# Kernel tuning notes

Measured on AMD Instinct MI355X. Metric: run time of the kernel, lower is better.

Reference implementation:

```python
import jax, jax.numpy as jnp
import numpy as np

N, E, F_IN, HID, H1, H2, H3, OUT = 10000, 160000, 50, 350, 4, 4, 6, 121


def _gat(x, src, dst, n, W, a_s, a_d, b, heads, C, concat):
    # PyG GATConv (dropout=0, eval): h = xW^T reshaped to [N,H,C]
    h = (x @ W.T).reshape(n, heads, C)
    alpha_src = jnp.einsum('nhc,hc->nh', h, a_s)  # [N,H]
    alpha_dst = jnp.einsum('nhc,hc->nh', h, a_d)  # [N,H]
    e = jax.nn.leaky_relu(alpha_src[src] + alpha_dst[dst], 0.2)  # [E,H]
    # numerically-stable segment softmax over incoming edges of each dst node
    m = jax.ops.segment_max(e, dst, num_segments=n)
    ee = jnp.exp(e - m[dst])
    s = jax.ops.segment_sum(ee, dst, num_segments=n)
    alpha = ee / s[dst]  # self-loops guarantee s > 0
    out = jax.ops.segment_sum(h[src] * alpha[:, :, None], dst, num_segments=n)  # [N,H,C]
    out = out.reshape(n, heads * C) if concat else out.mean(axis=1)
    return out + b


def setup_inputs() -> dict:
    key = jax.random.key(0)
    ks = jax.random.split(key, 16)
    sc = 0.05
    inp = {
        'x': jax.random.normal(ks[0], (N, F_IN), dtype=jnp.float32),
        'edge_index': jax.random.randint(ks[1], (2, E), 0, N, dtype=jnp.int64) if jax.config.jax_enable_x64 else jax.random.randint(ks[1], (2, E), 0, N, dtype=jnp.int32),
        'W1': jax.random.normal(ks[2], (H1 * HID, F_IN), dtype=jnp.float32) * sc,
        'a1s': jax.random.normal(ks[3], (H1, HID), dtype=jnp.float32) * sc,
        'a1d': jax.random.normal(ks[4], (H1, HID), dtype=jnp.float32) * sc,
        'b1': jnp.zeros((H1 * HID,), dtype=jnp.float32),
        'W2': jax.random.normal(ks[5], (H2 * HID, H1 * HID), dtype=jnp.float32) * sc,
        'a2s': jax.random.normal(ks[6], (H2, HID), dtype=jnp.float32) * sc,
        'a2d': jax.random.normal(ks[7], (H2, HID), dtype=jnp.float32) * sc,
        'b2': jnp.zeros((H2 * HID,), dtype=jnp.float32),
        'Wskip': jax.random.normal(ks[8], (H2 * HID, H1 * HID), dtype=jnp.float32) * sc,
        'W3': jax.random.normal(ks[9], (H3 * OUT, H2 * HID), dtype=jnp.float32) * sc,
        'a3s': jax.random.normal(ks[10], (H3, OUT), dtype=jnp.float32) * sc,
        'a3d': jax.random.normal(ks[11], (H3, OUT), dtype=jnp.float32) * sc,
        'b3': jnp.zeros((OUT,), dtype=jnp.float32),
    }
    return inp


def reference(x, edge_index, W1, a1s, a1d, b1, W2, a2s, a2d, b2, Wskip, W3, a3s, a3d, b3):
    n = x.shape[0]
    loops = jnp.arange(n, dtype=edge_index.dtype)  # PyG add_self_loops=True
    src = jnp.concatenate([edge_index[0], loops])
    dst = jnp.concatenate([edge_index[1], loops])
    h = jax.nn.elu(_gat(x, src, dst, n, W1, a1s, a1d, b1, H1, HID, True))
    x_in = h
    h = jax.nn.elu(_gat(h, src, dst, n, W2, a2s, a2d, b2, H2, HID, True))
    h = h + x_in @ Wskip.T  # skip connection (bias=False)
    return _gat(h, src, dst, n, W3, a3s, a3d, b3, H3, OUT, False)
```

## Files before the change

### kernel.cpp

```cpp
#include <hip/hip_runtime.h>
#include <math.h>

#define NNODES 10000
#define NEDGES 160000
#define E2 (NEDGES + NNODES)
#define F_IN 50
#define HIDC 350
#define NH1 4
#define NH2 4
#define NH3 6
#define OUTC 121
#define MAXE 96
#define KP1 64
#define KP2 1408
#define LD3 736
#define ROWSLACK 128

typedef __attribute__((ext_vector_type(8))) short short8;
typedef __attribute__((ext_vector_type(8))) unsigned short ushort8v;
typedef __attribute__((ext_vector_type(4))) float floatx4;

static __device__ __forceinline__ unsigned short f2bf(float f) {
    unsigned u = __float_as_uint(f);
    unsigned r = (u + 0x7fffu + ((u >> 16) & 1u)) >> 16;
    return (unsigned short)r;
}
static __device__ __forceinline__ float bf2f(unsigned short s) {
    return __uint_as_float(((unsigned)s) << 16);
}

#define GLL16(gp, lp)                                                      \
    __builtin_amdgcn_global_load_lds(                                      \
        (const __attribute__((address_space(1))) void*)(gp),               \
        (__attribute__((address_space(3))) void*)(lp), 16, 0, 0)

__global__ void count_kernel(const int* __restrict__ ei, int* __restrict__ cnt) {
    int i = blockIdx.x * blockDim.x + threadIdx.x;
    if (i >= E2) return;
    int dst = (i < NEDGES) ? ei[NEDGES + i] : (i - NEDGES);
    atomicAdd(&cnt[dst], 1);
}

__global__ void scan_kernel(const int* __restrict__ cnt, int* __restrict__ indptr,
                            int* __restrict__ cursor) {
    __shared__ int part[1024];
    int tid = threadIdx.x;
    const int CH = (NNODES + 1023) / 1024;
    int base = tid * CH;
    int s = 0;
    for (int i = 0; i < CH; i++) {
        int idx = base + i;
        if (idx < NNODES) s += cnt[idx];
    }
    part[tid] = s;
    __syncthreads();
    for (int off = 1; off < 1024; off <<= 1) {
        int v = (tid >= off) ? part[tid - off] : 0;
        __syncthreads();
        part[tid] += v;
        __syncthreads();
    }
    int run = (tid == 0) ? 0 : part[tid - 1];
    for (int i = 0; i < CH; i++) {
        int idx = base + i;
        if (idx < NNODES) {
            indptr[idx] = run;
            cursor[idx] = run;
            run += cnt[idx];
        }
    }
    if (tid == 0) indptr[NNODES] = part[1023];
}

__global__ void scatter_kernel(const int* __restrict__ ei, int* __restrict__ cursor,
                               int* __restrict__ esrc) {
    int i = blockIdx.x * blockDim.x + threadIdx.x;
    if (i >= E2) return;
    int src, dst;
    if (i < NEDGES) {
        src = ei[i];
        dst = ei[NEDGES + i];
    } else {
        src = dst = i - NEDGES;
    }
    int pos = atomicAdd(&cursor[dst], 1);
    esrc[pos] = src;
}

__global__ void splitW1_kernel(const float* __restrict__ W1,
                               unsigned short* __restrict__ w1Hi,
                               unsigned short* __restrict__ w1Lo) {
    int k = threadIdx.x;
    int r = blockIdx.x;
    float v = (k < F_IN) ? W1[(size_t)r * F_IN + k] : 0.f;
    unsigned short h = f2bf(v);
    w1Hi[(size_t)r * KP1 + k] = h;
    w1Lo[(size_t)r * KP1 + k] = f2bf(v - bf2f(h));
}

__global__ void splitB_kernel(const float* __restrict__ W2, const float* __restrict__ Wsk,
                              const float* __restrict__ W3,
                              unsigned short* __restrict__ w2Hi,
                              unsigned short* __restrict__ w3Hi) {
    int k = blockIdx.x * blockDim.x + threadIdx.x;
    if (k >= KP2) return;
    int r = blockIdx.y;
    const int K = 1400;
    const float* src;
    unsigned short* hi;
    int row;
    if (r < 1400) { src = W2; row = r; hi = w2Hi; }
    else if (r < 2800) { src = Wsk; row = r - 1400; hi = w2Hi + (size_t)1400 * KP2; }
    else { src = W3; row = r - 2800; hi = w3Hi; }
    float v = (k < K) ? src[(size_t)row * K + k] : 0.f;
    hi[(size_t)row * KP2 + k] = f2bf(v);
}

__global__ void atil_kernel(const float* __restrict__ W, const float* __restrict__ av_s,
                            const float* __restrict__ av_d, float* __restrict__ outS,
                            float* __restrict__ outD, int C, int K, int cchunk) {
    int k = blockIdx.x * 64 + (threadIdx.x & 63);
    if (k >= K) return;
    int h = blockIdx.y;
    int c0 = blockIdx.z * cchunk;
    int c1 = c0 + cchunk;
    if (c1 > C) c1 = C;
    float ss = 0.f, dd = 0.f;
    for (int c = c0; c < c1; c++) {
        float wv = W[((size_t)h * C + c) * K + k];
        ss = fmaf(wv, av_s[h * C + c], ss);
        dd = fmaf(wv, av_d[h * C + c], dd);
    }
    atomicAdd(&outS[(size_t)h * K + k], ss);
    atomicAdd(&outD[(size_t)h * K + k], dd);
}

__global__ void splitAT2_kernel(const float* __restrict__ atall,
                                unsigned short* __restrict__ atHi,
                                unsigned short* __restrict__ atLo) {
    int k = blockIdx.x * 64 + threadIdx.x;
    int r = blockIdx.y;
    float v = 0.f;
    if (k < 1400) {
        if (r < 4) v = atall[400 + r * 1400 + k];
        else if (r < 8) v = atall[6000 + (r - 4) * 1400 + k];
    }
    unsigned short h = f2bf(v);
    atHi[(size_t)r * KP2 + k] = h;
    atLo[(size_t)r * KP2 + k] = f2bf(v - bf2f(h));
}

__global__ __launch_bounds__(256) void alpha1x_kernel(const float* __restrict__ x,
                                                      const float* __restrict__ at1s,
                                                      const float* __restrict__ at1d,
                                                      float* __restrict__ as1,
                                                      float* __restrict__ ad1) {
    int wave = threadIdx.x >> 6, lane = threadIdx.x & 63;
    int n = blockIdx.x * 4 + wave;
    if (n >= NNODES) return;
    int kk = lane < F_IN ? lane : F_IN - 1;
    float v = (lane < F_IN) ? x[(size_t)n * F_IN + lane] : 0.f;
    float p[8];
#pragma unroll
    for (int h = 0; h < 4; h++) {
        p[h] = v * at1s[h * F_IN + kk];
        p[4 + h] = v * at1d[h * F_IN + kk];
    }
#pragma unroll
    for (int s = 0; s < 8; s++)
#pragma unroll
        for (int o = 32; o > 0; o >>= 1) p[s] += __shfl_xor(p[s], o, 64);
    if (lane == 0) {
#pragma unroll
        for (int h = 0; h < 4; h++) {
            as1[n * 4 + h] = p[h];
            ad1[n * 4 + h] = p[4 + h];
        }
    }
}

__global__ void zeropad_kernel(unsigned short* __restrict__ hi) {
    int i = blockIdx.x * 256 + threadIdx.x;
    if (i >= NNODES * 8) return;
    int n = i >> 3, c = 1400 + (i & 7);
    hi[(size_t)n * KP2 + c] = 0;
}

__global__ __launch_bounds__(256) void agg_x(
    const float* __restrict__ x, const float* __restrict__ as_n,
    const float* __restrict__ ad_n, const int* __restrict__ indptr,
    const int* __restrict__ esrc, unsigned short* __restrict__ xaggHi,
    unsigned short* __restrict__ xaggLo) {
    int n = blockIdx.x, tid = threadIdx.x;
    int s = indptr[n], e = indptr[n + 1];
    int deg = e - s;
    if (deg > MAXE) deg = MAXE;
    __shared__ int srcs[MAXE];
    __shared__ float wgt[MAXE * 4];

    if (tid < 64) {
        int lane = tid;
        float adv[4], mx[4], sm[4];
#pragma unroll
        for (int h = 0; h < 4; h++) {
            adv[h] = ad_n[n * 4 + h];
            mx[h] = -1e30f;
            sm[h] = 0.f;
        }
        for (int j = lane; j < deg; j += 64) {
            int sr = esrc[s + j];
            srcs[j] = sr;
#pragma unroll
            for (int h = 0; h < 4; h++) {
                float ev = as_n[sr * 4 + h] + adv[h];
                ev = ev > 0.f ? ev : 0.2f * ev;
                wgt[j * 4 + h] = ev;
                mx[h] = fmaxf(mx[h], ev);
            }
        }
#pragma unroll
        for (int h = 0; h < 4; h++)
#pragma unroll
            for (int o = 32; o > 0; o >>= 1) mx[h] = fmaxf(mx[h], __shfl_xor(mx[h], o, 64));
        for (int j = lane; j < deg; j += 64) {
#pragma unroll
            for (int h = 0; h < 4; h++) {
                float p = __expf(wgt[j * 4 + h] - mx[h]);
                wgt[j * 4 + h] = p;
                sm[h] += p;
            }
        }
#pragma unroll
        for (int h = 0; h < 4; h++) {
#pragma unroll
            for (int o = 32; o > 0; o >>= 1) sm[h] += __shfl_xor(sm[h], o, 64);
            sm[h] = 1.f / sm[h];
        }
        for (int j = lane; j < deg; j += 64) {
#pragma unroll
            for (int h = 0; h < 4; h++) wgt[j * 4 + h] *= sm[h];
        }
    }
    __syncthreads();

    int h = tid >> 6, k = tid & 63;
    float a = 0.f;
    if (k < F_IN) {
        float a2 = 0.f;
        int j = 0;
        for (; j + 1 < deg; j += 2) {
            a = fmaf(wgt[j * 4 + h], x[(size_t)srcs[j] * F_IN + k], a);
            a2 = fmaf(wgt[(j + 1) * 4 + h], x[(size_t)srcs[j + 1] * F_IN + k], a2);
        }
        if (j < deg) a = fmaf(wgt[j * 4 + h], x[(size_t)srcs[j] * F_IN + k], a);
        a += a2;
    }
    unsigned short hi = f2bf(a);
    xaggHi[(size_t)n * 256 + tid] = hi;
    xaggLo[(size_t)n * 256 + tid] = f2bf(a - bf2f(hi));
}

__global__ __launch_bounds__(256, 2) void gemm_h1(
    const unsigned short* __restrict__ xaggHi, const unsigned short* __restrict__ xaggLo,
    const unsigned short* __restrict__ w1Hi, const unsigned short* __restrict__ w1Lo,
    const float* __restrict__ bias, unsigned short* __restrict__ actHi) {
    __shared__ __align__(16) unsigned short sA[2][128 * 32];
    __shared__ __align__(16) unsigned short sB[2][256 * 32];
    int tid = threadIdx.x;
    int wave = tid >> 6, lane = tid & 63;
    int wm = (wave >> 1) * 64, wn = (wave & 1) * 128;
    int fr = lane & 15, kq = lane >> 4;
    int row0 = blockIdx.y * 128, col0 = blockIdx.x * 256;
    int hd = blockIdx.z;

    floatx4 acc[4][8];
#pragma unroll
    for (int i = 0; i < 4; i++)
#pragma unroll
        for (int j = 0; j < 8; j++)
#pragma unroll
            for (int q = 0; q < 4; q++) acc[i][j][q] = 0.f;

    int gpos = lane & 3;
    int rl = lane >> 2;
    int gsw = kq ^ ((fr >> 1) & 3);

    for (int k0 = 0; k0 < 64; k0 += 32) {
#pragma unroll
        for (int c = 0; c < 2; ++c) {
            int r = wave * 32 + c * 16 + rl;
            int g = gpos ^ ((r >> 1) & 3);
            size_t gofs = (size_t)(row0 + r) * 256 + hd * 64 + k0 + g * 8;
            size_t lofs = (size_t)r * 32 + (size_t)gpos * 8;
            GLL16(xaggHi + gofs, &sA[0][lofs]);
            GLL16(xaggLo + gofs, &sA[1][lofs]);
        }
#pragma unroll
        for (int c = 0; c < 4; ++c) {
            int r = wave * 64 + c * 16 + rl;
            int g = gpos ^ ((r >> 1) & 3);
            size_t gofs = (size_t)(hd * 350 + col0 + r) * KP1 + k0 + g * 8;
            size_t lofs = (size_t)r * 32 + (size_t)gpos * 8;
            GLL16(w1Hi + gofs, &sB[0][lofs]);
            GLL16(w1Lo + gofs, &sB[1][lofs]);
        }
        __syncthreads();

        short8 ah[4], al[4], bh[8], bl[8];
#pragma unroll
        for (int j = 0; j < 8; j++) {
            int rb = wn + j * 16 + fr;
            bh[j] = *(const short8*)&sB[0][rb * 32 + gsw * 8];
            bl[j] = *(const short8*)&sB[1][rb * 32 + gsw * 8];
        }
#pragma unroll
        for (int i = 0; i < 4; i++) {
            int ra = wm + i * 16 + fr;
            ah[i] = *(const short8*)&sA[0][ra * 32 + gsw * 8];
            al[i] = *(const short8*)&sA[1][ra * 32 + gsw * 8];
        }
#pragma unroll
        for (int i = 0; i < 4; i++)
#pragma unroll
            for (int j = 0; j < 8; j++) {
                acc[i][j] = __builtin_amdgcn_mfma_f32_16x16x32_bf16(ah[i], bh[j],
                                                                   acc[i][j], 0, 0, 0);
                acc[i][j] = __builtin_amdgcn_mfma_f32_16x16x32_bf16(al[i], bh[j],
                                                                   acc[i][j], 0, 0, 0);
                acc[i][j] = __builtin_amdgcn_mfma_f32_16x16x32_bf16(ah[i], bl[j],
                                                                   acc[i][j], 0, 0, 0);
            }
        __syncthreads();
    }

#pragma unroll
    for (int i = 0; i < 4; i++) {
#pragma unroll
        for (int rg = 0; rg < 4; rg++) {
            int rr = row0 + wm + i * 16 + kq * 4 + rg;
            if (rr >= NNODES) continue;
#pragma unroll
            for (int j = 0; j < 8; j++) {
                int cc = col0 + wn + j * 16 + fr;
                if (cc < 350) {
                    int gc = hd * 350 + cc;
                    float v = acc[i][j][rg] + bias[gc];
                    v = v > 0.f ? v : expm1f(v);
                    actHi[(size_t)rr * KP2 + gc] = f2bf(v);
                }
            }
        }
    }
}

__global__ __launch_bounds__(256) void alpha_mfma(
    const unsigned short* __restrict__ act, const unsigned short* __restrict__ tHi,
    const unsigned short* __restrict__ tLo, int H, float* __restrict__ asx,
    float* __restrict__ adx) {
    int wave = threadIdx.x >> 6, lane = threadIdx.x & 63;
    int row0 = (blockIdx.x * 4 + wave) * 16;
    if (row0 >= NNODES) return;
    int fr = lane & 15, kq = lane >> 4;
    floatx4 acc = {0.f, 0.f, 0.f, 0.f};
    const unsigned short* arow = act + (size_t)(row0 + fr) * KP2 + kq * 8;
    const unsigned short* brh = tHi + (size_t)fr * KP2 + kq * 8;
    const unsigned short* brl = tLo + (size_t)fr * KP2 + kq * 8;
#pragma unroll 4
    for (int k0 = 0; k0 < KP2; k0 += 32) {
        short8 a = *(const short8*)(arow + k0);
        short8 vh = *(const short8*)(brh + k0);
        short8 vl = *(const short8*)(brl + k0);
        acc = __builtin_amdgcn_mfma_f32_16x16x32_bf16(a, vh, acc, 0, 0, 0);
        acc = __builtin_amdgcn_mfma_f32_16x16x32_bf16(a, vl, acc, 0, 0, 0);
    }
#pragma unroll
    for (int rg = 0; rg < 4; rg++) {
        int rr = row0 + kq * 4 + rg;
        if (fr < H) asx[rr * H + fr] = acc[rg];
        else if (fr < 2 * H) adx[rr * H + (fr - H)] = acc[rg];
    }
}

template <int H>
__global__ __launch_bounds__(64) void alpha_edge(
    const float* __restrict__ as_n, const float* __restrict__ ad_n,
    const int* __restrict__ indptr, const int* __restrict__ esrc,
    float* __restrict__ walpha) {
    int n = blockIdx.x;
    int lane = threadIdx.x;
    int s = indptr[n], e = indptr[n + 1];
    int deg = e - s;
    if (deg > MAXE) deg = MAXE;
    __shared__ float wgt[MAXE * H];
    float adv[H], mx[H], sm[H];
#pragma unroll
    for (int h = 0; h < H; h++) {
        adv[h] = ad_n[n * H + h];
        mx[h] = -1e30f;
        sm[h] = 0.f;
    }
    for (int j = lane; j < deg; j += 64) {
        int sr = esrc[s + j];
#pragma unroll
        for (int h = 0; h < H; h++) {
            float ev = as_n[sr * H + h] + adv[h];
            ev = ev > 0.f ? ev : 0.2f * ev;
            wgt[j * H + h] = ev;
            mx[h] = fmaxf(mx[h], ev);
        }
    }
#pragma unroll
    for (int h = 0; h < H; h++)
#pragma unroll
        for (int o = 32; o > 0; o >>= 1) mx[h] = fmaxf(mx[h], __shfl_xor(mx[h], o, 64));
    for (int j = lane; j < deg; j += 64) {
#pragma unroll
        for (int h = 0; h < H; h++) {
            float p = __expf(wgt[j * H + h] - mx[h]);
            wgt[j * H + h] = p;
            sm[h] += p;
        }
    }
#pragma unroll
    for (int h = 0; h < H; h++) {
#pragma unroll
        for (int o = 32; o > 0; o >>= 1) sm[h] += __shfl_xor(sm[h], o, 64);
        sm[h] = 1.f / sm[h];
    }
    for (int j = lane; j < deg; j += 64) {
#pragma unroll
        for (int h = 0; h < H; h++) wgt[j * H + h] *= sm[h];
    }
    __syncthreads();
    for (int i = lane; i < deg * H; i += 64)
        walpha[(size_t)s * H + i] = wgt[i];
}

#define PH_MFMA(CH)                                                          \
    __builtin_amdgcn_s_barrier();                                            \
    asm volatile("s_waitcnt lgkmcnt(0)" ::: "memory");                       \
    __builtin_amdgcn_sched_barrier(0);                                       \
    __builtin_amdgcn_s_setprio(1);                                           \
    _Pragma("unroll")                                                        \
    for (int rf = 0; rf < 4; rf++) {                                         \
        _Pragma("unroll")                                                    \
        for (int cf = 0; cf < 4; cf++)                                       \
            acc[(CH) * 4 + rf][cf] = __builtin_amdgcn_mfma_f32_16x16x32_bf16( \
                a[rf], bfr[cf], acc[(CH) * 4 + rf][cf], 0, 0, 0);            \
    }                                                                        \
    __builtin_amdgcn_s_setprio(0);

__global__ __launch_bounds__(512, 2) void gemm_8p(
    const unsigned short* __restrict__ A, const unsigned short* __restrict__ B,
    unsigned short* __restrict__ Cb, int NN, int M, int Kp, int ldc) {
    __shared__ __align__(16) unsigned short sA[2][256 * 32];
    __shared__ __align__(16) unsigned short sB[2][256 * 32];
    int tid = threadIdx.x;
    int w = tid >> 6, lane = tid & 63;
    int wr = w >> 2, wc = w & 3;
    int fr = lane & 15, kq = lane >> 4;

    int gx = (int)gridDim.x;
    int nwg = gx * (int)gridDim.y;
    int bid = (int)blockIdx.y * gx + (int)blockIdx.x;
    int qq = nwg >> 3, rr8 = nwg & 7;
    int xcd = bid & 7, bdx = bid >> 3;
    int nb = (xcd < rr8) ? xcd * (qq + 1) + bdx : rr8 * (qq + 1) + (xcd - rr8) * qq + bdx;
    int row0 = (nb / gx) * 256, col0 = (nb % gx) * 256;

    floatx4 acc[8][4];
#pragma unroll
    for (int i = 0; i < 8; i++)
#pragma unroll
        for (int j = 0; j < 4; j++)
#pragma unroll
            for (int q = 0; q < 4; q++) acc[i][j][q] = 0.f;

    auto stage = [&](unsigned short* plane, const unsigned short* g, int rbase,
                     int kofs) {
#pragma unroll
        for (int l = 0; l < 2; l++) {
            int ix = l * 512 + tid, row = ix >> 2, sl = ix & 3;
            int gp = sl ^ ((row >> 1) & 3);
            GLL16(g + (size_t)(rbase + row) * Kp + kofs + gp * 8,
                  plane + (size_t)row * 32 + sl * 8);
        }
    };
    auto rdA = [&](const unsigned short* plane, int ch, short8* a) {
#pragma unroll
        for (int rf = 0; rf < 4; rf++) {
            int row = wr * 128 + ch * 64 + rf * 16 + fr;
            a[rf] = *(const short8*)(plane + (size_t)row * 32 +
                                     (size_t)(kq ^ ((row >> 1) & 3)) * 8);
        }
    };
    auto rdB = [&](const unsigned short* plane, short8* b) {
#pragma unroll
        for (int cf = 0; cf < 4; cf++) {
            int row = wc * 64 + cf * 16 + fr;
            b[cf] = *(const short8*)(plane + (size_t)row * 32 +
                                     (size_t)(kq ^ ((row >> 1) & 3)) * 8);
        }
    };

    const int nkt = Kp >> 6;
    stage(sA[0], A, row0, 0);
    stage(sB[0], B, col0, 0);
    stage(sB[1], B, col0, 32);
    asm volatile("s_waitcnt vmcnt(2)" ::: "memory");
    __builtin_amdgcn_sched_barrier(0);
    __builtin_amdgcn_s_barrier();

    short8 a[4], bfr[4];
    for (int t = 0; t < nkt; ++t) {
        int kt = t << 6;
        bool more = (t + 1 < nkt);
        rdA(sA[0], 0, a);
        rdB(sB[0], bfr);
        PH_MFMA(0)
        stage(sA[1], A, row0, kt + 32);
        __builtin_amdgcn_s_barrier();
        rdA(sA[0], 1, a);
        PH_MFMA(1)
        if (more) {
            stage(sB[0], B, col0, kt + 64);
            asm volatile("s_waitcnt vmcnt(2)" ::: "memory");
        } else {
            asm volatile("s_waitcnt vmcnt(0)" ::: "memory");
        }
        __builtin_amdgcn_sched_barrier(0);
        __builtin_amdgcn_s_barrier();
        rdA(sA[1], 0, a);
        rdB(sB[1], bfr);
        PH_MFMA(0)
        if (more) stage(sA[0], A, row0, kt + 64);
        __builtin_amdgcn_s_barrier();
        rdA(sA[1], 1, a);
        PH_MFMA(1)
        if (more) {
            stage(sB[1], B, col0, kt + 96);
            asm volatile("s_waitcnt vmcnt(2)" ::: "memory");
            __builtin_amdgcn_sched_barrier(0);
        }
        __builtin_amdgcn_s_barrier();
    }

#pragma unroll
    for (int ch = 0; ch < 2; ch++) {
#pragma unroll
        for (int rf = 0; rf < 4; rf++) {
#pragma unroll
            for (int rg = 0; rg < 4; rg++) {
                int rrow = row0 + wr * 128 + ch * 64 + rf * 16 + kq * 4 + rg;
                if (rrow >= NN) continue;
#pragma unroll
                for (int cf = 0; cf < 4; cf++) {
                    int cc = col0 + wc * 64 + cf * 16 + fr;
                    if (cc < M)
                        Cb[(size_t)rrow * ldc + cc] = f2bf(acc[ch * 4 + rf][cf][rg]);
                }
            }
        }
    }
}

__global__ __launch_bounds__(256, 2) void gemm_b16(
    const unsigned short* __restrict__ A, const unsigned short* __restrict__ B,
    unsigned short* __restrict__ Cb, int NN, int M, int Kp, int ldc) {
    __shared__ __align__(16) unsigned short sA[128 * 32];
    __shared__ __align__(16) unsigned short sB[256 * 32];
    int tid = threadIdx.x;
    int wave = tid >> 6, lane = tid & 63;
    int wm = (wave >> 1) * 64, wn = (wave & 1) * 128;
    int fr = lane & 15, kq = lane >> 4;

    int gx = (int)gridDim.x;
    int nwg = gx * (int)gridDim.y;
    int bid = (int)blockIdx.y * gx + (int)blockIdx.x;
    int qq = nwg >> 3, rr8 = nwg & 7;
    int xcd = bid & 7, idx = bid >> 3;
    int nb = (xcd < rr8) ? xcd * (qq + 1) + idx : rr8 * (qq + 1) + (xcd - rr8) * qq + idx;
    int row0 = (nb / gx) * 128, col0 = (nb % gx) * 256;

    floatx4 acc[4][8];
#pragma unroll
    for (int i = 0; i < 4; i++)
#pragma unroll
        for (int j = 0; j < 8; j++)
#pragma unroll
            for (int q = 0; q < 4; q++) acc[i][j][q] = 0.f;

    int gpos = lane & 3;
    int rl = lane >> 2;
    int gsw = kq ^ ((fr >> 1) & 3);

    for (int k0 = 0; k0 < Kp; k0 += 32) {
#pragma unroll
        for (int c = 0; c < 2; ++c) {
            int r = wave * 32 + c * 16 + rl;
            int g = gpos ^ ((r >> 1) & 3);
            GLL16(A + (size_t)(row0 + r) * Kp + k0 + g * 8,
                  &sA[(size_t)r * 32 + (size_t)gpos * 8]);
        }
#pragma unroll
        for (int c = 0; c < 4; ++c) {
            int r = wave * 64 + c * 16 + rl;
            int g = gpos ^ ((r >> 1) & 3);
            GLL16(B + (size_t)(col0 + r) * Kp + k0 + g * 8,
                  &sB[(size_t)r * 32 + (size_t)gpos * 8]);
        }
        __syncthreads();

        short8 ah[4], bh[8];
#pragma unroll
        for (int j = 0; j < 8; j++) {
            int rb = wn + j * 16 + fr;
            bh[j] = *(const short8*)&sB[rb * 32 + gsw * 8];
        }
#pragma unroll
        for (int i = 0; i < 4; i++) {
            int ra = wm + i * 16 + fr;
            ah[i] = *(const short8*)&sA[ra * 32 + gsw * 8];
        }
#pragma unroll
        for (int i = 0; i < 4; i++)
#pragma unroll
            for (int j = 0; j < 8; j++)
                acc[i][j] = __builtin_amdgcn_mfma_f32_16x16x32_bf16(ah[i], bh[j],
                                                                   acc[i][j], 0, 0, 0);
        __syncthreads();
    }

#pragma unroll
    for (int i = 0; i < 4; i++) {
#pragma unroll
        for (int rg = 0; rg < 4; rg++) {
            int rrow = row0 + wm + i * 16 + kq * 4 + rg;
            if (rrow >= NN) continue;
#pragma unroll
            for (int j = 0; j < 8; j++) {
                int cc = col0 + wn + j * 16 + fr;
                if (cc < M) Cb[(size_t)rrow * ldc + cc] = f2bf(acc[i][j][rg]);
            }
        }
    }
}

#define AGG_T 192
__global__ __launch_bounds__(AGG_T) void agg2(
    const unsigned short* __restrict__ hpreb, int ldh,
    const int* __restrict__ indptr, const int* __restrict__ esrc,
    const float* __restrict__ walpha, const float* __restrict__ bias,
    unsigned short* __restrict__ outHi, int Kp,
    const float* __restrict__ atns, const float* __restrict__ atnd,
    float* __restrict__ asx, float* __restrict__ adx) {
    constexpr int H = 4, C = 350, HC = 1400, HN = 6;
    int n = blockIdx.x;
    int tid = threadIdx.x;
    int s = indptr[n], e = indptr[n + 1];
    int deg = e - s;
    if (deg > MAXE) deg = MAXE;

    __shared__ int srcs[MAXE];
    __shared__ float wgt[MAXE * H];
    __shared__ float sAl[16];
    if (tid < 16) sAl[tid] = 0.f;
    for (int i = tid; i < deg; i += AGG_T) srcs[i] = esrc[s + i];
    for (int i = tid; i < deg * H; i += AGG_T) wgt[i] = walpha[(size_t)s * H + i];
    __syncthreads();

    constexpr int NV8 = HC / 8;
    float p[2 * HN];
#pragma unroll
    for (int q = 0; q < 2 * HN; q++) p[q] = 0.f;

    for (int c8 = tid; c8 < NV8; c8 += AGG_T) {
        int cb = c8 * 8;
        int h0 = cb / C;
        int sp = (h0 + 1) * C - cb;
        if (sp > 8) sp = 8;
        int h1 = (h0 + 1 < H) ? h0 + 1 : h0;
        float av[8];
#pragma unroll
        for (int q = 0; q < 8; q++) av[q] = 0.f;
        int j = 0;
        for (; j + 7 < deg; j += 8) {
            ushort8v v[8];
            float w0[8], w1[8];
#pragma unroll
            for (int t = 0; t < 8; t++)
                v[t] = *(const ushort8v*)(hpreb + (size_t)srcs[j + t] * ldh + cb);
#pragma unroll
            for (int t = 0; t < 8; t++) {
                w0[t] = wgt[(j + t) * H + h0];
                w1[t] = wgt[(j + t) * H + h1];
            }
#pragma unroll
            for (int t = 0; t < 8; t++)
#pragma unroll
                for (int q = 0; q < 8; q++)
                    av[q] = fmaf(q < sp ? w0[t] : w1[t], bf2f(v[t][q]), av[q]);
        }
        for (; j + 3 < deg; j += 4) {
            ushort8v v[4];
            float w0[4], w1[4];
#pragma unroll
            for (int t = 0; t < 4; t++)
                v[t] = *(const ushort8v*)(hpreb + (size_t)srcs[j + t] * ldh + cb);
#pragma unroll
            for (int t = 0; t < 4; t++) {
                w0[t] = wgt[(j + t) * H + h0];
                w1[t] = wgt[(j + t) * H + h1];
            }
#pragma unroll
            for (int t = 0; t < 4; t++)
#pragma unroll
                for (int q = 0; q < 8; q++)
                    av[q] = fmaf(q < sp ? w0[t] : w1[t], bf2f(v[t][q]), av[q]);
        }
        for (; j < deg; j++) {
            const ushort8v v0 = *(const ushort8v*)(hpreb + (size_t)srcs[j] * ldh + cb);
            float wa0 = wgt[j * H + h0], wa1 = wgt[j * H + h1];
#pragma unroll
            for (int q = 0; q < 8; q++) av[q] = fmaf(q < sp ? wa0 : wa1, bf2f(v0[q]), av[q]);
        }
#pragma unroll
        for (int q = 0; q < 8; q++) av[q] += bias[cb + q];
#pragma unroll
        for (int q = 0; q < 8; q++) av[q] = av[q] > 0.f ? av[q] : expm1f(av[q]);
        const ushort8v sk = *(const ushort8v*)(hpreb + (size_t)n * ldh + 1400 + cb);
#pragma unroll
        for (int q = 0; q < 8; q++) av[q] += bf2f(sk[q]);
#pragma unroll
        for (int h = 0; h < HN; h++) {
            float ss = 0.f, dd = 0.f;
#pragma unroll
            for (int q = 0; q < 8; q++) {
                ss = fmaf(av[q], atns[(size_t)h * HC + cb + q], ss);
                dd = fmaf(av[q], atnd[(size_t)h * HC + cb + q], dd);
            }
            p[h] += ss;
            p[HN + h] += dd;
        }
        ushort8v hi8;
#pragma unroll
        for (int q = 0; q < 8; q++) hi8[q] = f2bf(av[q]);
        *(ushort8v*)(outHi + (size_t)n * Kp + cb) = hi8;
    }
    for (int c = HC + tid; c < Kp; c += AGG_T) outHi[(size_t)n * Kp + c] = 0;
#pragma unroll
    for (int q = 0; q < 2 * HN; q++)
#pragma unroll
        for (int o = 32; o > 0; o >>= 1) p[q] += __shfl_xor(p[q], o, 64);
    if ((tid & 63) == 0) {
#pragma unroll
        for (int q = 0; q < 2 * HN; q++) atomicAdd(&sAl[q], p[q]);
    }
    __syncthreads();
    if (tid < HN) asx[n * HN + tid] = sAl[tid];
    else if (tid < 2 * HN) adx[n * HN + (tid - HN)] = sAl[tid];
}

template <int H, int C>
__global__ __launch_bounds__(AGG_T) void agg3(
    const unsigned short* __restrict__ hpreb, int ldh,
    const int* __restrict__ indptr, const int* __restrict__ esrc,
    const float* __restrict__ walpha, const float* __restrict__ bias,
    float* __restrict__ outF) {
    constexpr int HC = H * C;
    int n = blockIdx.x;
    int tid = threadIdx.x;
    int s = indptr[n], e = indptr[n + 1];
    int deg = e - s;
    if (deg > MAXE) deg = MAXE;

    __shared__ int srcs[MAXE];
    __shared__ float wgt[MAXE * H];
    __shared__ float aggsh[HC];
    for (int i = tid; i < deg; i += AGG_T) srcs[i] = esrc[s + i];
    for (int i = tid; i < deg * H; i += AGG_T) wgt[i] = walpha[(size_t)s * H + i];
    __syncthreads();

    constexpr int NV8 = (HC + 7) / 8;
    for (int c8 = tid; c8 < NV8; c8 += AGG_T) {
        int cb = c8 * 8;
        int h0 = cb / C;
        if (h0 >= H) h0 = H - 1;
        int sp = (h0 + 1) * C - cb;
        if (sp > 8) sp = 8;
        int h1 = (h0 + 1 < H) ? h0 + 1 : h0;
        float av[8];
#pragma unroll
        for (int q = 0; q < 8; q++) av[q] = 0.f;
        int j = 0;
        for (; j + 7 < deg; j += 8) {
            ushort8v v[8];
            float w0[8], w1[8];
#pragma unroll
            for (int t = 0; t < 8; t++)
                v[t] = *(const ushort8v*)(hpreb + (size_t)srcs[j + t] * ldh + cb);
#pragma unroll
            for (int t = 0; t < 8; t++) {
                w0[t] = wgt[(j + t) * H + h0];
                w1[t] = wgt[(j + t) * H + h1];
            }
#pragma unroll
            for (int t = 0; t < 8; t++)
#pragma unroll
                for (int q = 0; q < 8; q++)
                    av[q] = fmaf(q < sp ? w0[t] : w1[t], bf2f(v[t][q]), av[q]);
        }
        for (; j + 3 < deg; j += 4) {
            ushort8v v[4];
            float w0[4], w1[4];
#pragma unroll
            for (int t = 0; t < 4; t++)
                v[t] = *(const ushort8v*)(hpreb + (size_t)srcs[j + t] * ldh + cb);
#pragma unroll
            for (int t = 0; t < 4; t++) {
                w0[t] = wgt[(j + t) * H + h0];
                w1[t] = wgt[(j + t) * H + h1];
            }
#pragma unroll
            for (int t = 0; t < 4; t++)
#pragma unroll
                for (int q = 0; q < 8; q++)
                    av[q] = fmaf(q < sp ? w0[t] : w1[t], bf2f(v[t][q]), av[q]);
        }
        for (; j < deg; j++) {
            const ushort8v v0 = *(const ushort8v*)(hpreb + (size_t)srcs[j] * ldh + cb);
            float wa0 = wgt[j * H + h0], wa1 = wgt[j * H + h1];
#pragma unroll
            for (int q = 0; q < 8; q++) av[q] = fmaf(q < sp ? wa0 : wa1, bf2f(v0[q]), av[q]);
        }
#pragma unroll
        for (int q = 0; q < 8; q++)
            if (cb + q < HC) aggsh[cb + q] = av[q];
    }
    __syncthreads();
    for (int c = tid; c < C; c += AGG_T) {
        float sres = 0.f;
#pragma unroll
        for (int h = 0; h < H; h++) sres += aggsh[h * C + c];
        outF[(size_t)n * C + c] = sres * (1.f / (float)H) + bias[c];
    }
}

extern "C" void kernel_launch(void* const* d_in, const int* in_sizes, int n_in,
                              void* d_out, int out_size, void* d_ws, size_t ws_size,
                              hipStream_t stream) {
    const float* x = (const float*)d_in[0];
    const int* ei = (const int*)d_in[1];
    const float* W1 = (const float*)d_in[2];
    const float* a1s = (const float*)d_in[3];
    const float* a1d = (const float*)d_in[4];
    const float* b1 = (const float*)d_in[5];
    const float* W2 = (const float*)d_in[6];
    const float* a2s = (const float*)d_in[7];
    const float* a2d = (const float*)d_in[8];
    const float* b2 = (const float*)d_in[9];
    const float* Wsk = (const float*)d_in[10];
    const float* W3 = (const float*)d_in[11];
    const float* a3s = (const float*)d_in[12];
    const float* a3d = (const float*)d_in[13];
    const float* b3 = (const float*)d_in[14];
    float* out = (float*)d_out;

    char* w = (char*)d_ws;
    size_t off = 0;
    auto alloc = [&](size_t bytes) -> char* {
        char* p = w + off;
        off += (bytes + 255) & ~(size_t)255;
        return p;
    };
    unsigned short* hpreb = (unsigned short*)alloc((size_t)(NNODES + ROWSLACK) * 2800 * 2);
    unsigned short* actHi = (unsigned short*)alloc((size_t)(NNODES + 384) * KP2 * 2);
    unsigned short* xaggHi = (unsigned short*)alloc((size_t)(NNODES + ROWSLACK) * 256 * 2);
    unsigned short* xaggLo = (unsigned short*)alloc((size_t)(NNODES + ROWSLACK) * 256 * 2);
    unsigned short* w1Hi = (unsigned short*)alloc((size_t)(1400 + 512) * KP1 * 2);
    unsigned short* w1Lo = (unsigned short*)alloc((size_t)(1400 + 512) * KP1 * 2);
    unsigned short* w2Hi = (unsigned short*)alloc((size_t)(2800 + ROWSLACK) * KP2 * 2);
    unsigned short* w3Hi = (unsigned short*)alloc((size_t)(726 + ROWSLACK) * KP2 * 2);
    unsigned short* at2Hi = (unsigned short*)alloc((size_t)16 * KP2 * 2);
    unsigned short* at2Lo = (unsigned short*)alloc((size_t)16 * KP2 * 2);
    float* atall = (float*)alloc((size_t)28400 * 4);
    int* cnt = (int*)alloc((size_t)(NNODES + 16) * 4);
    float* at1s = atall;
    float* at1d = atall + 200;
    float* at2s = atall + 400;
    float* at2d = atall + 6000;
    float* at3s = atall + 11600;
    float* at3d = atall + 20000;
    float* asP = (float*)alloc((size_t)NNODES * 6 * 4);
    float* adP = (float*)alloc((size_t)NNODES * 6 * 4);
    float* asQ = (float*)alloc((size_t)NNODES * 6 * 4);
    float* adQ = (float*)alloc((size_t)NNODES * 6 * 4);
    int* indptr = (int*)alloc((size_t)(NNODES + 16) * 4);
    int* cursor = (int*)alloc((size_t)(NNODES + 16) * 4);
    int* esrc = (int*)alloc((size_t)E2 * 4);
    float* walpha = (float*)alloc((size_t)E2 * 6 * 4);

    size_t zbytes = (size_t)((char*)cnt - (char*)atall) + (NNODES + 16) * 4;
    hipMemsetAsync(atall, 0, zbytes, stream);

    splitW1_kernel<<<1400, 64, 0, stream>>>(W1, w1Hi, w1Lo);
    splitB_kernel<<<dim3(6, 2800 + 726), 256, 0, stream>>>(W2, Wsk, W3, w2Hi, w3Hi);
    atil_kernel<<<dim3(1, 4, 5), 64, 0, stream>>>(W1, a1s, a1d, at1s, at1d, HIDC, F_IN, 70);
    atil_kernel<<<dim3(22, 4, 5), 64, 0, stream>>>(W2, a2s, a2d, at2s, at2d, HIDC, 1400, 70);
    atil_kernel<<<dim3(22, 6, 4), 64, 0, stream>>>(W3, a3s, a3d, at3s, at3d, OUTC, 1400, 31);
    splitAT2_kernel<<<dim3(22, 16), 64, 0, stream>>>(atall, at2Hi, at2Lo);
    alpha1x_kernel<<<(NNODES + 3) / 4, 256, 0, stream>>>(x, at1s, at1d, asP, adP);

    count_kernel<<<(E2 + 255) / 256, 256, 0, stream>>>(ei, cnt);
    scan_kernel<<<1, 1024, 0, stream>>>(cnt, indptr, cursor);
    scatter_kernel<<<(E2 + 255) / 256, 256, 0, stream>>>(ei, cursor, esrc);

    zeropad_kernel<<<(NNODES * 8 + 255) / 256, 256, 0, stream>>>(actHi);

    dim3 blk(256);
    int gy = (NNODES + 127) / 128;

    agg_x<<<NNODES, 256, 0, stream>>>(x, asP, adP, indptr, esrc, xaggHi, xaggLo);
    gemm_h1<<<dim3(2, gy, 4), blk, 0, stream>>>(xaggHi, xaggLo, w1Hi, w1Lo, b1, actHi);
    alpha_mfma<<<(NNODES / 16 + 3) / 4, 256, 0, stream>>>(actHi, at2Hi, at2Lo, 4, asQ, adQ);
    alpha_edge<4><<<NNODES, 64, 0, stream>>>(asQ, adQ, indptr, esrc, walpha);

    {
        int M = 2800;
        dim3 grid((M + 255) / 256, (NNODES + 255) / 256);
        gemm_8p<<<grid, 512, 0, stream>>>(actHi, w2Hi, hpreb, NNODES, M, KP2, 2800);
        agg2<<<NNODES, AGG_T, 0, stream>>>(hpreb, 2800, indptr, esrc, walpha, b2,
                                           actHi, KP2, at3s, at3d, asP, adP);
    }
    {
        alpha_edge<6><<<NNODES, 64, 0, stream>>>(asP, adP, indptr, esrc, walpha);
        int M = NH3 * OUTC;
        dim3 grid((M + 255) / 256, gy);
        gemm_b16<<<grid, blk, 0, stream>>>(actHi, w3Hi, hpreb, NNODES, M, KP2, LD3);
        agg3<NH3, OUTC><<<NNODES, AGG_T, 0, stream>>>(
            hpreb, LD3, indptr, esrc, walpha, b3, out);
    }
}
```

Measured before the change: 616.4 us.

## Split layer-2 aggregation into two half-row blocks per node with partial-alpha reduction

The layer-2 aggregation kernel now launches two 128-thread blocks per node, each covering 704 of the 1400 (padded to 1408) bf16 columns, instead of one 192-thread block per node. The 192-thread version left many threads idle in a second pass over 175 vectors. Each half writes its partial layer-3 attention dot products to a scratch buffer, and a small new kernel sums the two halves into asx/adx. This doubles the edge-index and weight staging per node and adds an extra kernel launch, in exchange for better thread utilisation and more parallelism.

```diff
diff --git a/kernel.cpp b/kernel.cpp
--- a/kernel.cpp
+++ b/kernel.cpp
@@ -646,16 +646,16 @@
     }
 }
 
-#define AGG_T 192
-__global__ __launch_bounds__(AGG_T) void agg2(
+__global__ __launch_bounds__(128) void agg2h(
     const unsigned short* __restrict__ hpreb, int ldh,
     const int* __restrict__ indptr, const int* __restrict__ esrc,
     const float* __restrict__ walpha, const float* __restrict__ bias,
     unsigned short* __restrict__ outHi, int Kp,
     const float* __restrict__ atns, const float* __restrict__ atnd,
-    float* __restrict__ asx, float* __restrict__ adx) {
+    float* __restrict__ a3part) {
     constexpr int H = 4, C = 350, HC = 1400, HN = 6;
-    int n = blockIdx.x;
+    int n = blockIdx.x >> 1;
+    int hf = blockIdx.x & 1;
     int tid = threadIdx.x;
     int s = indptr[n], e = indptr[n + 1];
     int deg = e - s;
@@ -663,104 +663,122 @@
 
     __shared__ int srcs[MAXE];
     __shared__ float wgt[MAXE * H];
-    __shared__ float sAl[16];
-    if (tid < 16) sAl[tid] = 0.f;
-    for (int i = tid; i < deg; i += AGG_T) srcs[i] = esrc[s + i];
-    for (int i = tid; i < deg * H; i += AGG_T) wgt[i] = walpha[(size_t)s * H + i];
+    __shared__ float pred[2][12];
+    for (int i = tid; i < deg; i += 128) srcs[i] = esrc[s + i];
+    for (int i = tid; i < deg * H; i += 128) wgt[i] = walpha[(size_t)s * H + i];
     __syncthreads();
 
-    constexpr int NV8 = HC / 8;
     float p[2 * HN];
 #pragma unroll
     for (int q = 0; q < 2 * HN; q++) p[q] = 0.f;
 
-    for (int c8 = tid; c8 < NV8; c8 += AGG_T) {
-        int cb = c8 * 8;
-        int h0 = cb / C;
-        int sp = (h0 + 1) * C - cb;
-        if (sp > 8) sp = 8;
-        int h1 = (h0 + 1 < H) ? h0 + 1 : h0;
-        float av[8];
-#pragma unroll
-        for (int q = 0; q < 8; q++) av[q] = 0.f;
-        int j = 0;
-        for (; j + 7 < deg; j += 8) {
-            ushort8v v[8];
-            float w0[8], w1[8];
-#pragma unroll
-            for (int t = 0; t < 8; t++)
-                v[t] = *(const ushort8v*)(hpreb + (size_t)srcs[j + t] * ldh + cb);
-#pragma unroll
-            for (int t = 0; t < 8; t++) {
-                w0[t] = wgt[(j + t) * H + h0];
-                w1[t] = wgt[(j + t) * H + h1];
-            }
-#pragma unroll
-            for (int t = 0; t < 8; t++)
+    if (tid < 88) {
+        int cb = hf * 704 + tid * 8;
+        if (cb < HC) {
+            int h0 = cb / C;
+            int sp = (h0 + 1) * C - cb;
+            if (sp > 8) sp = 8;
+            int h1 = (h0 + 1 < H) ? h0 + 1 : h0;
+            float av[8];
+#pragma unroll
+            for (int q = 0; q < 8; q++) av[q] = 0.f;
+            int j = 0;
+            for (; j + 7 < deg; j += 8) {
+                ushort8v v[8];
+                float w0[8], w1[8];
+#pragma unroll
+                for (int t = 0; t < 8; t++)
+                    v[t] = *(const ushort8v*)(hpreb + (size_t)srcs[j + t] * ldh + cb);
+#pragma unroll
+                for (int t = 0; t < 8; t++) {
+                    w0[t] = wgt[(j + t) * H + h0];
+                    w1[t] = wgt[(j + t) * H + h1];
+                }
+#pragma unroll
+                for (int t = 0; t < 8; t++)
+#pragma unroll
+                    for (int q = 0; q < 8; q++)
+                        av[q] = fmaf(q < sp ? w0[t] : w1[t], bf2f(v[t][q]), av[q]);
+            }
+            for (; j + 3 < deg; j += 4) {
+                ushort8v v[4];
+                float w0[4], w1[4];
+#pragma unroll
+                for (int t = 0; t < 4; t++)
+                    v[t] = *(const ushort8v*)(hpreb + (size_t)srcs[j + t] * ldh + cb);
+#pragma unroll
+                for (int t = 0; t < 4; t++) {
+                    w0[t] = wgt[(j + t) * H + h0];
+                    w1[t] = wgt[(j + t) * H + h1];
+                }
+#pragma unroll
+                for (int t = 0; t < 4; t++)
+#pragma unroll
+                    for (int q = 0; q < 8; q++)
+                        av[q] = fmaf(q < sp ? w0[t] : w1[t], bf2f(v[t][q]), av[q]);
+            }
+            for (; j < deg; j++) {
+                const ushort8v v0 = *(const ushort8v*)(hpreb + (size_t)srcs[j] * ldh + cb);
+                float wa0 = wgt[j * H + h0], wa1 = wgt[j * H + h1];
 #pragma unroll
                 for (int q = 0; q < 8; q++)
-                    av[q] = fmaf(q < sp ? w0[t] : w1[t], bf2f(v[t][q]), av[q]);
-        }
-        for (; j + 3 < deg; j += 4) {
-            ushort8v v[4];
-            float w0[4], w1[4];
-#pragma unroll
-            for (int t = 0; t < 4; t++)
-                v[t] = *(const ushort8v*)(hpreb + (size_t)srcs[j + t] * ldh + cb);
-#pragma unroll
-            for (int t = 0; t < 4; t++) {
-                w0[t] = wgt[(j + t) * H + h0];
-                w1[t] = wgt[(j + t) * H + h1];
-            }
-#pragma unroll
-            for (int t = 0; t < 4; t++)
-#pragma unroll
-                for (int q = 0; q < 8; q++)
-                    av[q] = fmaf(q < sp ? w0[t] : w1[t], bf2f(v[t][q]), av[q]);
-        }
-        for (; j < deg; j++) {
-            const ushort8v v0 = *(const ushort8v*)(hpreb + (size_t)srcs[j] * ldh + cb);
-            float wa0 = wgt[j * H + h0], wa1 = wgt[j * H + h1];
-#pragma unroll
-            for (int q = 0; q < 8; q++) av[q] = fmaf(q < sp ? wa0 : wa1, bf2f(v0[q]), av[q]);
-        }
-#pragma unroll
-        for (int q = 0; q < 8; q++) av[q] += bias[cb + q];
-#pragma unroll
-        for (int q = 0; q < 8; q++) av[q] = av[q] > 0.f ? av[q] : expm1f(av[q]);
-        const ushort8v sk = *(const ushort8v*)(hpreb + (size_t)n * ldh + 1400 + cb);
-#pragma unroll
-        for (int q = 0; q < 8; q++) av[q] += bf2f(sk[q]);
-#pragma unroll
-        for (int h = 0; h < HN; h++) {
-            float ss = 0.f, dd = 0.f;
-#pragma unroll
-            for (int q = 0; q < 8; q++) {
-                ss = fmaf(av[q], atns[(size_t)h * HC + cb + q], ss);
-                dd = fmaf(av[q], atnd[(size_t)h * HC + cb + q], dd);
-            }
-            p[h] += ss;
-            p[HN + h] += dd;
-        }
-        ushort8v hi8;
-#pragma unroll
-        for (int q = 0; q < 8; q++) hi8[q] = f2bf(av[q]);
-        *(ushort8v*)(outHi + (size_t)n * Kp + cb) = hi8;
-    }
-    for (int c = HC + tid; c < Kp; c += AGG_T) outHi[(size_t)n * Kp + c] = 0;
+                    av[q] = fmaf(q < sp ? wa0 : wa1, bf2f(v0[q]), av[q]);
+            }
+#pragma unroll
+            for (int q = 0; q < 8; q++) av[q] += bias[cb + q];
+#pragma unroll
+            for (int q = 0; q < 8; q++) av[q] = av[q] > 0.f ? av[q] : expm1f(av[q]);
+            const ushort8v sk = *(const ushort8v*)(hpreb + (size_t)n * ldh + 1400 + cb);
+#pragma unroll
+            for (int q = 0; q < 8; q++) av[q] += bf2f(sk[q]);
+#pragma unroll
+            for (int h = 0; h < HN; h++) {
+                float ss = 0.f, dd = 0.f;
+#pragma unroll
+                for (int q = 0; q < 8; q++) {
+                    ss = fmaf(av[q], atns[(size_t)h * HC + cb + q], ss);
+                    dd = fmaf(av[q], atnd[(size_t)h * HC + cb + q], dd);
+                }
+                p[h] += ss;
+                p[HN + h] += dd;
+            }
+            ushort8v hi8;
+#pragma unroll
+            for (int q = 0; q < 8; q++) hi8[q] = f2bf(av[q]);
+            *(ushort8v*)(outHi + (size_t)n * Kp + cb) = hi8;
+        } else {
+            ushort8v z;
+#pragma unroll
+            for (int q = 0; q < 8; q++) z[q] = 0;
+            *(ushort8v*)(outHi + (size_t)n * Kp + cb) = z;
+        }
+    }
 #pragma unroll
     for (int q = 0; q < 2 * HN; q++)
 #pragma unroll
         for (int o = 32; o > 0; o >>= 1) p[q] += __shfl_xor(p[q], o, 64);
+    int wid = tid >> 6;
     if ((tid & 63) == 0) {
 #pragma unroll
-        for (int q = 0; q < 2 * HN; q++) atomicAdd(&sAl[q], p[q]);
+        for (int q = 0; q < 2 * HN; q++) pred[wid][q] = p[q];
     }
     __syncthreads();
-    if (tid < HN) asx[n * HN + tid] = sAl[tid];
-    else if (tid < 2 * HN) adx[n * HN + (tid - HN)] = sAl[tid];
-}
-
+    if (tid < 2 * HN)
+        a3part[(size_t)(n * 2 + hf) * 12 + tid] = pred[0][tid] + pred[1][tid];
+}
+
+__global__ __launch_bounds__(256) void a3r(const float* __restrict__ a3part,
+                                           float* __restrict__ asx,
+                                           float* __restrict__ adx) {
+    int t = blockIdx.x * 256 + threadIdx.x;
+    if (t >= NNODES * 12) return;
+    int n = t / 12, q = t - n * 12;
+    float v = a3part[(size_t)(n * 2) * 12 + q] + a3part[(size_t)(n * 2 + 1) * 12 + q];
+    if (q < 6) asx[n * 6 + q] = v;
+    else adx[n * 6 + (q - 6)] = v;
+}
+
+#define AGG_T 192
 template <int H, int C>
 __global__ __launch_bounds__(AGG_T) void agg3(
     const unsigned short* __restrict__ hpreb, int ldh,
@@ -899,6 +917,7 @@
     int* cursor = (int*)alloc((size_t)(NNODES + 16) * 4);
     int* esrc = (int*)alloc((size_t)E2 * 4);
     float* walpha = (float*)alloc((size_t)E2 * 6 * 4);
+    float* a3part = (float*)alloc((size_t)NNODES * 24 * 4);
 
     size_t zbytes = (size_t)((char*)cnt - (char*)atall) + (NNODES + 16) * 4;
     hipMemsetAsync(atall, 0, zbytes, stream);
@@ -929,8 +948,9 @@
         int M = 2800;
         dim3 grid((M + 255) / 256, (NNODES + 255) / 256);
         gemm_8p<<<grid, 512, 0, stream>>>(actHi, w2Hi, hpreb, NNODES, M, KP2, 2800);
-        agg2<<<NNODES, AGG_T, 0, stream>>>(hpreb, 2800, indptr, esrc, walpha, b2,
-                                           actHi, KP2, at3s, at3d, asP, adP);
+        agg2h<<<NNODES * 2, 128, 0, stream>>>(hpreb, 2800, indptr, esrc, walpha, b2,
+                                              actHi, KP2, at3s, at3d, a3part);
+        a3r<<<(NNODES * 12 + 255) / 256, 256, 0, stream>>>(a3part, asP, adP);
     }
     {
         alpha_edge<6><<<NNODES, 64, 0, stream>>>(asP, adP, indptr, esrc, walpha);
```

Result: slower. 629.6 us (+2.1%).
